# Optimization experiments

Measured on AMD Instinct MI355X. Metric: run time of the kernel, lower is better.

Reference implementation:

```python
import jax, jax.numpy as jnp
import numpy as np

VOCAB = 100000
BEO = 512
BATCH = 2048
SEQ = 50
MEAN = 0.0
STD = 1.0


def _linear_params(key, fan_in, fan_out):
    k1, k2 = jax.random.split(key)
    bound = 1.0 / np.sqrt(fan_in)
    W = jax.random.uniform(k1, (fan_in, fan_out), jnp.float32, -bound, bound)
    b = jax.random.uniform(k2, (fan_out,), jnp.float32, -bound, bound)
    return W, b


def setup_inputs() -> dict:
    key = jax.random.key(0)
    ks = jax.random.split(key, 8)
    s = jax.random.randint(ks[0], (BATCH, SEQ), 0, VOCAB, dtype=jnp.int64)
    x = jax.random.normal(ks[1], (BATCH, BEO), dtype=jnp.float32)
    W_bow_h, b_bow_h = _linear_params(ks[2], VOCAB, 256)
    W_bow_pred, b_bow_pred = _linear_params(ks[3], 256, 5)
    W_bow_embd, b_bow_embd = _linear_params(ks[4], 256, 64)
    W_beo_h, b_beo_h = _linear_params(ks[5], BEO, 256)
    W_beo_pred, b_beo_pred = _linear_params(ks[6], 256, 5)
    W_beo_embd, b_beo_embd = _linear_params(ks[7], 256, 64)
    return {
        "s": s, "x": x,
        "W_bow_h": W_bow_h, "b_bow_h": b_bow_h,
        "W_bow_pred": W_bow_pred, "b_bow_pred": b_bow_pred,
        "W_bow_embd": W_bow_embd, "b_bow_embd": b_bow_embd,
        "W_beo_h": W_beo_h, "b_beo_h": b_beo_h,
        "W_beo_pred": W_beo_pred, "b_beo_pred": b_beo_pred,
        "W_beo_embd": W_beo_embd, "b_beo_embd": b_beo_embd,
    }


def reference(s, x,
              W_bow_h, b_bow_h, W_bow_pred, b_bow_pred, W_bow_embd, b_bow_embd,
              W_beo_h, b_beo_h, W_beo_pred, b_beo_pred, W_beo_embd, b_beo_embd):
    B = s.shape[0]
    xn = (x - MEAN) / STD
    # multi-hot: scatter_ sets 1 regardless of duplicates (set, not add)
    rows = jnp.arange(B)[:, None]  # [B,1] broadcasts against s [B,SEQ]
    bow = jnp.zeros((B, VOCAB), jnp.float32).at[rows, s].set(1.0)
    bow_h = jax.nn.leaky_relu(bow @ W_bow_h + b_bow_h, 0.2)  # [B,256]
    beo_h = jax.nn.leaky_relu(xn @ W_beo_h + b_beo_h, 0.2)   # [B,256]
    bow_p = bow_h @ W_bow_pred + b_bow_pred  # [B,5]
    beo_p = beo_h @ W_beo_pred + b_beo_pred  # [B,5]
    bow_e = bow_h @ W_bow_embd + b_bow_embd  # [B,64]
    beo_e = beo_h @ W_beo_embd + b_beo_embd  # [B,64]
    return (bow_e, beo_e, bow_p, beo_p)
```

## Files before the change

### kernel.cpp

```cpp
#include <hip/hip_runtime.h>
#include <cstdint>

#define VOCAB 100000
#define NB    2048
#define SEQ   50
#define HID   256
#define XIN   512
#define NE    64
#define NP    5

#define OFF_BOW_E 0
#define OFF_BEO_E (NB*NE)
#define OFF_BOW_P (2*NB*NE)
#define OFF_BEO_P (2*NB*NE + NB*NP)

#define BOW_T   1024
#define BOW_W   16
#define BOW_TPW 4

__global__ __launch_bounds__(BOW_T, 4) void bow_kernel(
    const int*   __restrict__ s,   const float* __restrict__ Wbh,
    const float* __restrict__ bbh,
    const float* __restrict__ Wbp, const float* __restrict__ bbp,
    const float* __restrict__ Wbe, const float* __restrict__ bbe,
    float* __restrict__ out)
{
    __shared__ float part[BOW_W*HID];
    __shared__ float h[HID];
    const int tid  = threadIdx.x;
    const int row  = blockIdx.x;
    const int lane = tid & 63;
    const int w    = tid >> 6;
    const int* srow = s + row*SEQ;

    int tokl = (lane < SEQ) ? srow[lane] : -3;

    int   tk[BOW_TPW];
    float mk[BOW_TPW];
    #pragma unroll
    for (int ii = 0; ii < BOW_TPW; ++ii) {
        const int i = w + BOW_W*ii;
        int t = (i < SEQ) ? srow[i] : -3;
        t = __builtin_amdgcn_readfirstlane(t);
        unsigned long long dup = __ballot(lane < i && tokl == t);
        mk[ii] = (t >= 0 && dup == 0ull) ? 1.0f : 0.0f;
        tk[ii] = (t < 0) ? 0 : t;
    }

    float4 v[BOW_TPW];
    const float* wbase = Wbh + (size_t)lane*4;
    #pragma unroll
    for (int ii = 0; ii < BOW_TPW; ++ii)
        v[ii] = *(const float4*)(wbase + (size_t)tk[ii]*HID);
    __builtin_amdgcn_sched_barrier(0);

    float ax=0.f, ay=0.f, az=0.f, aw_=0.f;
    #pragma unroll
    for (int ii = 0; ii < BOW_TPW; ++ii) {
        ax = fmaf(mk[ii], v[ii].x, ax);
        ay = fmaf(mk[ii], v[ii].y, ay);
        az = fmaf(mk[ii], v[ii].z, az);
        aw_= fmaf(mk[ii], v[ii].w, aw_);
    }
    *(float4*)&part[w*HID + lane*4] = make_float4(ax, ay, az, aw_);
    __syncthreads();

    if (tid < HID) {
        float hv = bbh[tid];
        #pragma unroll
        for (int p = 0; p < BOW_W; ++p) hv += part[p*HID + tid];
        hv = hv > 0.f ? hv : 0.2f*hv;
        h[tid] = hv;
    }
    __syncthreads();

    {
        const int jj = tid & 63, p2 = tid >> 6;
        float ps = 0.f;
        #pragma unroll
        for (int kk = 0; kk < 16; ++kk) {
            int k = p2*16 + kk;
            ps = fmaf(h[k], Wbe[k*NE + jj], ps);
        }
        part[tid] = ps;
    }
    float pp = 0.f;
    if (tid < 8*NP) {
        const int p = tid / NP, jj = tid % NP;
        #pragma unroll 8
        for (int kk = 0; kk < 32; ++kk) {
            int k = p*32 + kk;
            pp = fmaf(h[k], Wbp[k*NP + jj], pp);
        }
    }
    __syncthreads();
    if (tid < NE) {
        float e = bbe[tid];
        #pragma unroll
        for (int p2 = 0; p2 < 16; ++p2) e += part[p2*64 + tid];
        out[OFF_BOW_E + (size_t)row*NE + tid] = e;
    }
    __syncthreads();
    if (tid < 8*NP) part[tid] = pp;
    __syncthreads();
    if (tid < NP) {
        float sp = bbp[tid];
        #pragma unroll
        for (int q = 0; q < 8; ++q) sp += part[q*NP + tid];
        out[OFF_BOW_P + (size_t)row*NP + tid] = sp;
    }
}

#define BEO_BLOCKS 256
#define BEO_ROWS   8

__global__ __launch_bounds__(256, 1) void beo_kernel(
    const float* __restrict__ x,
    const float* __restrict__ Weh, const float* __restrict__ beh,
    const float* __restrict__ Wep, const float* __restrict__ bep,
    const float* __restrict__ Wee, const float* __restrict__ bee,
    float* __restrict__ out)
{
    __shared__ float xs[BEO_ROWS*XIN];
    const int tid = threadIdx.x;
    const int r0  = blockIdx.x * BEO_ROWS;
    {
        const float4* src = (const float4*)(x + (size_t)r0 * XIN);
        float4*       dst = (float4*)xs;
        #pragma unroll
        for (int i = 0; i < (BEO_ROWS*XIN/4)/256; ++i)
            dst[i*256 + tid] = src[i*256 + tid];
    }
    __syncthreads();

    float acc[BEO_ROWS];
    {
        float bv = beh[tid];
        #pragma unroll
        for (int r = 0; r < BEO_ROWS; ++r) acc[r] = bv;
    }
    const float4* xs4 = (const float4*)xs;
    #pragma unroll 2
    for (int k4 = 0; k4 < XIN/4; ++k4) {
        const float* wcol = Weh + (size_t)(4*k4)*HID + tid;
        float w0 = wcol[0];
        float w1 = wcol[HID];
        float w2 = wcol[2*HID];
        float w3 = wcol[3*HID];
        #pragma unroll
        for (int r = 0; r < BEO_ROWS; ++r) {
            float4 xv = xs4[r*(XIN/4) + k4];
            acc[r] = fmaf(xv.x, w0, acc[r]);
            acc[r] = fmaf(xv.y, w1, acc[r]);
            acc[r] = fmaf(xv.z, w2, acc[r]);
            acc[r] = fmaf(xv.w, w3, acc[r]);
        }
    }
    __syncthreads();
    float* hs = xs;
    #pragma unroll
    for (int r = 0; r < BEO_ROWS; ++r) {
        float vv = acc[r];
        hs[r*HID + tid] = vv > 0.f ? vv : 0.2f*vv;
    }
    __syncthreads();

    {
        const int jj = tid & 63;
        const int r  = tid >> 6;
        const float4* hs4 = (const float4*)hs;
        float s0 = 0.f, s1 = 0.f;
        #pragma unroll 4
        for (int k4 = 0; k4 < HID/4; ++k4) {
            float4 ha = hs4[r*(HID/4) + k4];
            float4 hb = hs4[(r+4)*(HID/4) + k4];
            const float* wp = Wee + (size_t)(4*k4)*NE + jj;
            float w0 = wp[0], w1 = wp[NE], w2 = wp[2*NE], w3 = wp[3*NE];
            s0 = fmaf(ha.x, w0, s0); s0 = fmaf(ha.y, w1, s0);
            s0 = fmaf(ha.z, w2, s0); s0 = fmaf(ha.w, w3, s0);
            s1 = fmaf(hb.x, w0, s1); s1 = fmaf(hb.y, w1, s1);
            s1 = fmaf(hb.z, w2, s1); s1 = fmaf(hb.w, w3, s1);
        }
        float bias = bee[jj];
        out[OFF_BEO_E + (size_t)(r0+r)*NE   + jj] = s0 + bias;
        out[OFF_BEO_E + (size_t)(r0+r+4)*NE + jj] = s1 + bias;
    }
    if (tid < BEO_ROWS*NP) {
        const int r = tid / NP, jj = tid % NP;
        float sp = bep[jj];
        for (int k = 0; k < HID; ++k)
            sp = fmaf(hs[r*HID + k], Wep[k*NP + jj], sp);
        out[OFF_BEO_P + (size_t)(r0+r)*NP + jj] = sp;
    }
}

extern "C" void kernel_launch(void* const* d_in, const int* in_sizes, int n_in,
                              void* d_out, int out_size, void* d_ws, size_t ws_size,
                              hipStream_t stream) {
    const int*   s   = (const int*)  d_in[0];
    const float* x   = (const float*)d_in[1];
    const float* Wbh = (const float*)d_in[2];
    const float* bbh = (const float*)d_in[3];
    const float* Wbp = (const float*)d_in[4];
    const float* bbp = (const float*)d_in[5];
    const float* Wbe = (const float*)d_in[6];
    const float* bbe = (const float*)d_in[7];
    const float* Weh = (const float*)d_in[8];
    const float* beh = (const float*)d_in[9];
    const float* Wep = (const float*)d_in[10];
    const float* bep = (const float*)d_in[11];
    const float* Wee = (const float*)d_in[12];
    const float* bee = (const float*)d_in[13];
    float* out = (float*)d_out;

    bow_kernel<<<dim3(NB), dim3(BOW_T), 0, stream>>>(
        s, Wbh, bbh, Wbp, bbp, Wbe, bbe, out);
    beo_kernel<<<dim3(BEO_BLOCKS), dim3(256), 0, stream>>>(
        x, Weh, beh, Wep, bep, Wee, bee, out);
}
```

Baseline: 241.3 us.

## Double-buffer beo weight tiles into LDS via async global_load_lds

The beo kernel is restructured to handle 4 rows per block, which gives 512 blocks instead of 256. It streams W_beo_h tiles of 32 k-rows into double-buffered LDS with global_load_lds, so the next tile loads while the current one is computed. x is stored transposed in LDS so each k step reads one float4 covering 4 rows. The bow gather is rewritten in inline asm so the four dwordx4 loads are issued back to back before a single wait. The trade-off is that each block now rereads the full weight matrix for fewer rows, roughly doubling global weight traffic, and the asm loads limit what the compiler can schedule.

```diff
diff --git a/kernel.cpp b/kernel.cpp
--- a/kernel.cpp
+++ b/kernel.cpp
@@ -1,5 +1,7 @@
 #include <hip/hip_runtime.h>
 #include <cstdint>
+
+typedef float f32x4 __attribute__((ext_vector_type(4)));
 
 #define VOCAB 100000
 #define NB    2048
@@ -13,6 +15,9 @@
 #define OFF_BEO_E (NB*NE)
 #define OFF_BOW_P (2*NB*NE)
 #define OFF_BEO_P (2*NB*NE + NB*NP)
+
+#define AS1(p) ((const __attribute__((address_space(1))) void*)(p))
+#define AS3(p) ((__attribute__((address_space(3))) void*)(p))
 
 #define BOW_T   1024
 #define BOW_W   16
@@ -47,21 +52,29 @@
         tk[ii] = (t < 0) ? 0 : t;
     }
 
-    float4 v[BOW_TPW];
     const float* wbase = Wbh + (size_t)lane*4;
-    #pragma unroll
-    for (int ii = 0; ii < BOW_TPW; ++ii)
-        v[ii] = *(const float4*)(wbase + (size_t)tk[ii]*HID);
+    const float* a0 = wbase + (size_t)tk[0]*HID;
+    const float* a1 = wbase + (size_t)tk[1]*HID;
+    const float* a2 = wbase + (size_t)tk[2]*HID;
+    const float* a3 = wbase + (size_t)tk[3]*HID;
+    f32x4 v0, v1, v2, v3;
+    asm volatile("global_load_dwordx4 %0, %1, off" : "=v"(v0) : "v"(a0));
+    asm volatile("global_load_dwordx4 %0, %1, off" : "=v"(v1) : "v"(a1));
+    asm volatile("global_load_dwordx4 %0, %1, off" : "=v"(v2) : "v"(a2));
+    asm volatile("global_load_dwordx4 %0, %1, off" : "=v"(v3) : "v"(a3));
+    asm volatile("s_waitcnt vmcnt(0)" ::: "memory");
     __builtin_amdgcn_sched_barrier(0);
 
     float ax=0.f, ay=0.f, az=0.f, aw_=0.f;
-    #pragma unroll
-    for (int ii = 0; ii < BOW_TPW; ++ii) {
-        ax = fmaf(mk[ii], v[ii].x, ax);
-        ay = fmaf(mk[ii], v[ii].y, ay);
-        az = fmaf(mk[ii], v[ii].z, az);
-        aw_= fmaf(mk[ii], v[ii].w, aw_);
-    }
+    ax = fmaf(mk[0], v0[0], ax); ay = fmaf(mk[0], v0[1], ay);
+    az = fmaf(mk[0], v0[2], az); aw_= fmaf(mk[0], v0[3], aw_);
+    ax = fmaf(mk[1], v1[0], ax); ay = fmaf(mk[1], v1[1], ay);
+    az = fmaf(mk[1], v1[2], az); aw_= fmaf(mk[1], v1[3], aw_);
+    ax = fmaf(mk[2], v2[0], ax); ay = fmaf(mk[2], v2[1], ay);
+    az = fmaf(mk[2], v2[2], az); aw_= fmaf(mk[2], v2[3], aw_);
+    ax = fmaf(mk[3], v3[0], ax); ay = fmaf(mk[3], v3[1], ay);
+    az = fmaf(mk[3], v3[2], az); aw_= fmaf(mk[3], v3[3], aw_);
+
     *(float4*)&part[w*HID + lane*4] = make_float4(ax, ay, az, aw_);
     __syncthreads();
 
@@ -111,81 +124,101 @@
     }
 }
 
-#define BEO_BLOCKS 256
-#define BEO_ROWS   8
-
-__global__ __launch_bounds__(256, 1) void beo_kernel(
+#define BEO_RPB 4
+#define BEO_BK  32
+#define BEO_NT  (XIN/BEO_BK)
+#define BEO_GRID (NB/BEO_RPB)
+
+__global__ __launch_bounds__(256, 2) void beo_kernel(
     const float* __restrict__ x,
     const float* __restrict__ Weh, const float* __restrict__ beh,
     const float* __restrict__ Wep, const float* __restrict__ bep,
     const float* __restrict__ Wee, const float* __restrict__ bee,
     float* __restrict__ out)
 {
-    __shared__ float xs[BEO_ROWS*XIN];
-    const int tid = threadIdx.x;
-    const int r0  = blockIdx.x * BEO_ROWS;
+    __shared__ float Wlds[2][BEO_BK*HID];
+    __shared__ float xT[XIN*BEO_RPB];
+    const int tid  = threadIdx.x;
+    const int lane = tid & 63;
+    const int w    = tid >> 6;
+    const int r0   = blockIdx.x * BEO_RPB;
+
     {
-        const float4* src = (const float4*)(x + (size_t)r0 * XIN);
-        float4*       dst = (float4*)xs;
-        #pragma unroll
-        for (int i = 0; i < (BEO_ROWS*XIN/4)/256; ++i)
-            dst[i*256 + tid] = src[i*256 + tid];
-    }
-    __syncthreads();
-
-    float acc[BEO_ROWS];
+        float a0 = x[(size_t)(r0+0)*XIN + tid];
+        float a1 = x[(size_t)(r0+1)*XIN + tid];
+        float a2 = x[(size_t)(r0+2)*XIN + tid];
+        float a3 = x[(size_t)(r0+3)*XIN + tid];
+        float b0 = x[(size_t)(r0+0)*XIN + 256 + tid];
+        float b1 = x[(size_t)(r0+1)*XIN + 256 + tid];
+        float b2 = x[(size_t)(r0+2)*XIN + 256 + tid];
+        float b3 = x[(size_t)(r0+3)*XIN + 256 + tid];
+        *(f32x4*)&xT[(size_t)tid*4]       = (f32x4){a0,a1,a2,a3};
+        *(f32x4*)&xT[(size_t)(256+tid)*4] = (f32x4){b0,b1,b2,b3};
+    }
+
+    auto stage = [&](int t, int b) {
+        const size_t tbase = (size_t)t * BEO_BK * HID;
+        #pragma unroll
+        for (int j = 0; j < 8; ++j) {
+            const int off = j*1024 + w*256;
+            __builtin_amdgcn_global_load_lds(
+                AS1(Weh + tbase + off + lane*4),
+                AS3(&Wlds[b][off]), 16, 0, 0);
+        }
+    };
+
+    stage(0, 0);
+    asm volatile("s_waitcnt vmcnt(0)" ::: "memory");
+    __syncthreads();
+
+    float acc0=0.f, acc1=0.f, acc2=0.f, acc3=0.f;
+    int buf = 0;
+    for (int t = 0; t < BEO_NT; ++t) {
+        if (t+1 < BEO_NT) stage(t+1, buf^1);
+        const float* wl = &Wlds[buf][0];
+        const f32x4* xt = (const f32x4*)&xT[(size_t)t*BEO_BK*4];
+        #pragma unroll 8
+        for (int k = 0; k < BEO_BK; ++k) {
+            float wv = wl[k*HID + tid];
+            f32x4 xv = xt[k];
+            acc0 = fmaf(xv[0], wv, acc0);
+            acc1 = fmaf(xv[1], wv, acc1);
+            acc2 = fmaf(xv[2], wv, acc2);
+            acc3 = fmaf(xv[3], wv, acc3);
+        }
+        asm volatile("s_waitcnt vmcnt(0)" ::: "memory");
+        __syncthreads();
+        buf ^= 1;
+    }
+
+    float bv = beh[tid];
+    float h0 = acc0 + bv; h0 = h0 > 0.f ? h0 : 0.2f*h0;
+    float h1 = acc1 + bv; h1 = h1 > 0.f ? h1 : 0.2f*h1;
+    float h2 = acc2 + bv; h2 = h2 > 0.f ? h2 : 0.2f*h2;
+    float h3 = acc3 + bv; h3 = h3 > 0.f ? h3 : 0.2f*h3;
+    float* hs = xT;
+    hs[0*HID + tid] = h0;
+    hs[1*HID + tid] = h1;
+    hs[2*HID + tid] = h2;
+    hs[3*HID + tid] = h3;
+    __syncthreads();
+
     {
-        float bv = beh[tid];
-        #pragma unroll
-        for (int r = 0; r < BEO_ROWS; ++r) acc[r] = bv;
-    }
-    const float4* xs4 = (const float4*)xs;
-    #pragma unroll 2
-    for (int k4 = 0; k4 < XIN/4; ++k4) {
-        const float* wcol = Weh + (size_t)(4*k4)*HID + tid;
-        float w0 = wcol[0];
-        float w1 = wcol[HID];
-        float w2 = wcol[2*HID];
-        float w3 = wcol[3*HID];
-        #pragma unroll
-        for (int r = 0; r < BEO_ROWS; ++r) {
-            float4 xv = xs4[r*(XIN/4) + k4];
-            acc[r] = fmaf(xv.x, w0, acc[r]);
-            acc[r] = fmaf(xv.y, w1, acc[r]);
-            acc[r] = fmaf(xv.z, w2, acc[r]);
-            acc[r] = fmaf(xv.w, w3, acc[r]);
-        }
-    }
-    __syncthreads();
-    float* hs = xs;
-    #pragma unroll
-    for (int r = 0; r < BEO_ROWS; ++r) {
-        float vv = acc[r];
-        hs[r*HID + tid] = vv > 0.f ? vv : 0.2f*vv;
-    }
-    __syncthreads();
-
-    {
-        const int jj = tid & 63;
-        const int r  = tid >> 6;
-        const float4* hs4 = (const float4*)hs;
-        float s0 = 0.f, s1 = 0.f;
+        const int jj = tid & 63, r = tid >> 6;
+        const f32x4* h4 = (const f32x4*)&hs[r*HID];
+        float s0 = 0.f;
         #pragma unroll 4
         for (int k4 = 0; k4 < HID/4; ++k4) {
-            float4 ha = hs4[r*(HID/4) + k4];
-            float4 hb = hs4[(r+4)*(HID/4) + k4];
+            f32x4 hv = h4[k4];
             const float* wp = Wee + (size_t)(4*k4)*NE + jj;
-            float w0 = wp[0], w1 = wp[NE], w2 = wp[2*NE], w3 = wp[3*NE];
-            s0 = fmaf(ha.x, w0, s0); s0 = fmaf(ha.y, w1, s0);
-            s0 = fmaf(ha.z, w2, s0); s0 = fmaf(ha.w, w3, s0);
-            s1 = fmaf(hb.x, w0, s1); s1 = fmaf(hb.y, w1, s1);
-            s1 = fmaf(hb.z, w2, s1); s1 = fmaf(hb.w, w3, s1);
-        }
-        float bias = bee[jj];
-        out[OFF_BEO_E + (size_t)(r0+r)*NE   + jj] = s0 + bias;
-        out[OFF_BEO_E + (size_t)(r0+r+4)*NE + jj] = s1 + bias;
-    }
-    if (tid < BEO_ROWS*NP) {
+            s0 = fmaf(hv[0], wp[0],    s0);
+            s0 = fmaf(hv[1], wp[NE],   s0);
+            s0 = fmaf(hv[2], wp[2*NE], s0);
+            s0 = fmaf(hv[3], wp[3*NE], s0);
+        }
+        out[OFF_BEO_E + (size_t)(r0+r)*NE + jj] = s0 + bee[jj];
+    }
+    if (tid < BEO_RPB*NP) {
         const int r = tid / NP, jj = tid % NP;
         float sp = bep[jj];
         for (int k = 0; k < HID; ++k)
@@ -215,6 +248,6 @@
 
     bow_kernel<<<dim3(NB), dim3(BOW_T), 0, stream>>>(
         s, Wbh, bbh, Wbp, bbp, Wbe, bbe, out);
-    beo_kernel<<<dim3(BEO_BLOCKS), dim3(256), 0, stream>>>(
+    beo_kernel<<<dim3(BEO_GRID), dim3(256), 0, stream>>>(
         x, Weh, beh, Wep, bep, Wee, bee, out);
 }
```

New measurement: 232.2 us. -3.8%, faster.
